# Kernel optimization log

Measured on AMD Instinct MI355X. Metric: run time of the kernel, lower is better.

Reference implementation:

```python
import jax, jax.numpy as jnp
import numpy as np

KF, KD, STRIDE, PAD = 5, 3, 1, 2  # filter width, depth, stride, padding from cfg
N, C, H, W = 256, 3, 224, 224


def setup_inputs() -> dict:
    key = jax.random.key(0)
    k1, k2, k3 = jax.random.split(key, 3)
    bound = 1.0 / np.sqrt(KF * KF * KD)  # nn.Linear default init bound
    x = jax.random.normal(k1, (N, C, H, W), dtype=jnp.float32)
    W_lin = jax.random.uniform(k2, (1, KF * KF * KD), dtype=jnp.float32, minval=-bound, maxval=bound)
    b = jax.random.uniform(k3, (1,), dtype=jnp.float32, minval=-bound, maxval=bound)
    return {"x": x, "W_lin": W_lin, "b": b}


def reference(x, W_lin, b):
    # Linear over patches flattened in (C, Kh, Kw) order == conv with OIHW kernel.
    w = W_lin.reshape(1, KD, KF, KF)  # [O=1, I=3, Kh=5, Kw=5]
    out = jax.lax.conv_general_dilated(
        x, w,
        window_strides=(STRIDE, STRIDE),
        padding=[(PAD, PAD), (PAD, PAD)],
        dimension_numbers=("NCHW", "OIHW", "NCHW"),
    )  # [N, 1, H, W]
    out = out + b  # bias broadcast
    return out[:, 0, :, :]  # module returns [N, W, H] with W == H
```

## Files before the change

### kernel.cpp

```cpp
#include <hip/hip_runtime.h>


namespace {

constexpr int Hc = 224, Wc = 224, Cc = 3;
constexpr int HW = Hc * Wc;
constexpr int CHW = Cc * HW;
constexpr int BAND = 16;
constexpr int SROWS = BAND + 4;
constexpr int RST = 232;
constexpr int BUFD = SROWS * RST;
constexpr int SPI = Hc / BAND;
constexpr int BLK = 256;

__device__ __forceinline__ void gl_lds16(const float* g, float* l) {
  __builtin_amdgcn_global_load_lds(
      (const __attribute__((address_space(1))) void*)g,
      (__attribute__((address_space(3))) void*)l, 16, 0, 0);
}

__global__ __launch_bounds__(BLK) void conv5x5_r21(
    const float* __restrict__ x, const float* __restrict__ wl,
    const float* __restrict__ bptr, float* __restrict__ out) {
  __shared__ __align__(16) float sm[2 * BUFD];

  const int tid = threadIdx.x;
  const int lane = tid & 63;
  const int wv = tid >> 6;

  const int cpx = gridDim.x >> 3;
  const int bid = (blockIdx.x & 7) * cpx + (blockIdx.x >> 3);
  const int n = bid / SPI;
  const int band = bid % SPI;

  float w[Cc][5][5];
#pragma unroll
  for (int c = 0; c < Cc; ++c)
#pragma unroll
    for (int i = 0; i < 25; ++i) w[c][i / 5][i % 5] = wl[c * 25 + i];
  const float bias = bptr[0];

  const float* xn = x + (size_t)n * CHW;
  float* outn = out + (size_t)n * HW;

  const int g = tid & 31;
  const int tg = tid >> 5;
  const bool lo = (g == 0), hi = (g == 31);
  const int rdo = g * 7 + 2;

  float acc[2][7];

#define STAGE_P(P)                                                            \
  do {                                                                        \
    const float* gch_ = xn + (size_t)(P) * HW;                                \
    float* smb_ = sm + ((P) & 1) * BUFD;                                      \
    _Pragma("unroll") for (int i_ = 0; i_ < 5; ++i_) {                        \
      const int r_ = wv + 4 * i_;                                             \
      const int gy_ = band * BAND - 2 + r_;                                   \
      float* ld_ = smb_ + r_ * RST + 4;                                       \
      if (gy_ >= 0 && gy_ < Hc) {                                             \
        if (lane < 56)                                                        \
          gl_lds16(gch_ + (size_t)gy_ * Wc + lane * 4, ld_);                  \
      } else {                                                                \
        if (lane < 56)                                                        \
          *(float4*)(ld_ + lane * 4) = make_float4(0.f, 0.f, 0.f, 0.f);       \
      }                                                                       \
    }                                                                         \
  } while (0)

#define COMPUTE_P(P)                                                          \
  do {                                                                        \
    constexpr int ch_ = (P);                                                  \
    const float* smb_ = sm + ((P) & 1) * BUFD;                                \
    if (ch_ == 0) {                                                           \
      _Pragma("unroll") for (int r_ = 0; r_ < 2; ++r_)                        \
          _Pragma("unroll") for (int c_ = 0; c_ < 7; ++c_)                    \
              acc[r_][c_] = 0.f;                                              \
    }                                                                         \
    _Pragma("unroll") for (int jj_ = 0; jj_ < 6; ++jj_) {                     \
      const float* rp_ = smb_ + (tg * 2 + jj_) * RST + rdo;                   \
      float win_[11];                                                         \
      _Pragma("unroll") for (int j_ = 0; j_ < 11; ++j_) win_[j_] = rp_[j_];   \
      win_[0] = lo ? 0.f : win_[0];                                           \
      win_[1] = lo ? 0.f : win_[1];                                           \
      win_[9] = hi ? 0.f : win_[9];                                           \
      win_[10] = hi ? 0.f : win_[10];                                         \
      _Pragma("unroll") for (int r_ = 0; r_ < 2; ++r_) {                      \
        if (r_ <= jj_ && jj_ - r_ <= 4) {                                     \
          _Pragma("unroll") for (int kx_ = 0; kx_ < 5; ++kx_) {               \
            const float wv_ = w[ch_][jj_ - r_][kx_];                          \
            _Pragma("unroll") for (int c_ = 0; c_ < 7; ++c_) {                \
              acc[r_][c_] = fmaf(win_[c_ + kx_], wv_, acc[r_][c_]);           \
            }                                                                 \
          }                                                                   \
        }                                                                     \
      }                                                                       \
    }                                                                         \
    if (ch_ == 2) {                                                           \
      _Pragma("unroll") for (int r_ = 0; r_ < 2; ++r_) {                      \
        const int gy_ = band * BAND + tg * 2 + r_;                            \
        float* op_ = outn + (size_t)gy_ * Wc + g * 7;                         \
        _Pragma("unroll") for (int c_ = 0; c_ < 7; ++c_)                      \
            op_[c_] = acc[r_][c_] + bias;                                     \
      }                                                                       \
    }                                                                         \
  } while (0)

  STAGE_P(0);
  __syncthreads(); STAGE_P(1); COMPUTE_P(0);
  __syncthreads(); STAGE_P(2); COMPUTE_P(1);
  __syncthreads();             COMPUTE_P(2);

#undef STAGE_P
#undef COMPUTE_P
}

}

extern "C" void kernel_launch(void* const* d_in, const int* in_sizes, int n_in,
                              void* d_out, int out_size, void* d_ws, size_t ws_size,
                              hipStream_t stream) {
  const float* x  = (const float*)d_in[0];
  const float* wl = (const float*)d_in[1];
  const float* b  = (const float*)d_in[2];
  float* out = (float*)d_out;

  const int N = out_size / HW;
  const int nblk = N * SPI;

  conv5x5_r21<<<nblk, BLK, 0, stream>>>(x, wl, b, out);
}
```

Before: 42.54 us.

## Process two bands per block with a six-stage pipeline and pre-zeroed halo

Each block now handles two consecutive 16-row bands, so the double-buffered channel pipeline runs six stages instead of three and is primed once per two bands. Grid size is halved. The left and right halo columns in shared memory are zeroed once up front, which removes the per-window lo/hi selects in the inner loop. Compute sections are wrapped in s_setprio to raise wave priority during the FMAs. The tradeoff is fewer blocks for latency hiding and a dependence on the staging loads never overwriting the zeroed halo columns.

Measured after the change: 47.89 us. 1.13x slower.

```diff
diff --git a/kernel.cpp b/kernel.cpp
--- a/kernel.cpp
+++ b/kernel.cpp
@@ -10,7 +10,7 @@
 constexpr int SROWS = BAND + 4;
 constexpr int RST = 232;
 constexpr int BUFD = SROWS * RST;
-constexpr int SPI = Hc / BAND;
+constexpr int CPI = 7;
 constexpr int BLK = 256;
 
 __device__ __forceinline__ void gl_lds16(const float* g, float* l) {
@@ -19,7 +19,7 @@
       (__attribute__((address_space(3))) void*)l, 16, 0, 0);
 }
 
-__global__ __launch_bounds__(BLK) void conv5x5_r21(
+__global__ __launch_bounds__(BLK) void conv5x5_r23(
     const float* __restrict__ x, const float* __restrict__ wl,
     const float* __restrict__ bptr, float* __restrict__ out) {
   __shared__ __align__(16) float sm[2 * BUFD];
@@ -30,8 +30,8 @@
 
   const int cpx = gridDim.x >> 3;
   const int bid = (blockIdx.x & 7) * cpx + (blockIdx.x >> 3);
-  const int n = bid / SPI;
-  const int band = bid % SPI;
+  const int n = bid / CPI;
+  const int b0 = (bid % CPI) * 2;
 
   float w[Cc][5][5];
 #pragma unroll
@@ -45,18 +45,27 @@
 
   const int g = tid & 31;
   const int tg = tid >> 5;
-  const bool lo = (g == 0), hi = (g == 31);
   const int rdo = g * 7 + 2;
 
   float acc[2][7];
 
+  if (tid < 160) {
+    const int buf = tid / 80;
+    const int rem = tid % 80;
+    const int row = rem >> 2;
+    const int j = rem & 3;
+    const int dw = (j < 2) ? (2 + j) : (226 + j);
+    sm[buf * BUFD + row * RST + dw] = 0.f;
+  }
+
 #define STAGE_P(P)                                                            \
   do {                                                                        \
-    const float* gch_ = xn + (size_t)(P) * HW;                                \
+    const int band_ = b0 + (P) / 3;                                           \
+    const float* gch_ = xn + (size_t)((P) % 3) * HW;                          \
     float* smb_ = sm + ((P) & 1) * BUFD;                                      \
     _Pragma("unroll") for (int i_ = 0; i_ < 5; ++i_) {                        \
       const int r_ = wv + 4 * i_;                                             \
-      const int gy_ = band * BAND - 2 + r_;                                   \
+      const int gy_ = band_ * BAND - 2 + r_;                                  \
       float* ld_ = smb_ + r_ * RST + 4;                                       \
       if (gy_ >= 0 && gy_ < Hc) {                                             \
         if (lane < 56)                                                        \
@@ -70,21 +79,19 @@
 
 #define COMPUTE_P(P)                                                          \
   do {                                                                        \
-    constexpr int ch_ = (P);                                                  \
+    constexpr int ch_ = (P) % 3;                                              \
+    const int band_ = b0 + (P) / 3;                                           \
     const float* smb_ = sm + ((P) & 1) * BUFD;                                \
     if (ch_ == 0) {                                                           \
       _Pragma("unroll") for (int r_ = 0; r_ < 2; ++r_)                        \
           _Pragma("unroll") for (int c_ = 0; c_ < 7; ++c_)                    \
               acc[r_][c_] = 0.f;                                              \
     }                                                                         \
+    __builtin_amdgcn_s_setprio(1);                                            \
     _Pragma("unroll") for (int jj_ = 0; jj_ < 6; ++jj_) {                     \
       const float* rp_ = smb_ + (tg * 2 + jj_) * RST + rdo;                   \
       float win_[11];                                                         \
       _Pragma("unroll") for (int j_ = 0; j_ < 11; ++j_) win_[j_] = rp_[j_];   \
-      win_[0] = lo ? 0.f : win_[0];                                           \
-      win_[1] = lo ? 0.f : win_[1];                                           \
-      win_[9] = hi ? 0.f : win_[9];                                           \
-      win_[10] = hi ? 0.f : win_[10];                                         \
       _Pragma("unroll") for (int r_ = 0; r_ < 2; ++r_) {                      \
         if (r_ <= jj_ && jj_ - r_ <= 4) {                                     \
           _Pragma("unroll") for (int kx_ = 0; kx_ < 5; ++kx_) {               \
@@ -96,9 +103,10 @@
         }                                                                     \
       }                                                                       \
     }                                                                         \
+    __builtin_amdgcn_s_setprio(0);                                            \
     if (ch_ == 2) {                                                           \
       _Pragma("unroll") for (int r_ = 0; r_ < 2; ++r_) {                      \
-        const int gy_ = band * BAND + tg * 2 + r_;                            \
+        const int gy_ = band_ * BAND + tg * 2 + r_;                           \
         float* op_ = outn + (size_t)gy_ * Wc + g * 7;                         \
         _Pragma("unroll") for (int c_ = 0; c_ < 7; ++c_)                      \
             op_[c_] = acc[r_][c_] + bias;                                     \
@@ -109,7 +117,10 @@
   STAGE_P(0);
   __syncthreads(); STAGE_P(1); COMPUTE_P(0);
   __syncthreads(); STAGE_P(2); COMPUTE_P(1);
-  __syncthreads();             COMPUTE_P(2);
+  __syncthreads(); STAGE_P(3); COMPUTE_P(2);
+  __syncthreads(); STAGE_P(4); COMPUTE_P(3);
+  __syncthreads(); STAGE_P(5); COMPUTE_P(4);
+  __syncthreads();             COMPUTE_P(5);
 
 #undef STAGE_P
 #undef COMPUTE_P
@@ -126,7 +137,7 @@
   float* out = (float*)d_out;
 
   const int N = out_size / HW;
-  const int nblk = N * SPI;
+  const int nblk = N * CPI;
 
-  conv5x5_r21<<<nblk, BLK, 0, stream>>>(x, wl, b, out);
+  conv5x5_r23<<<nblk, BLK, 0, stream>>>(x, wl, b, out);
 }
```

## Give each wavefront its own 4-row slice with private LDS buffers, no block barriers

Applied to the files above, without the earlier changes.

Restructures the conv so each 64-lane wavefront owns a 4-output-row slice with a private double-buffered LDS region. Barrier-based staging is replaced by manual vmcnt/lgkmcnt waits, so waves never synchronise with each other. Halo rows are loaded with clamped addresses and then zeroed for edge slices, and the left/right padding columns are zeroed once in LDS instead of per-window selects. Vertical halo overhead rises from 4 extra rows per 16 to 4 per 4, which increases global load traffic, and correctness now depends on hand-written wait counts.

New measurement: 44.38 us. +4.3%, slower.

```diff
diff --git a/kernel.cpp b/kernel.cpp
--- a/kernel.cpp
+++ b/kernel.cpp
@@ -6,12 +6,11 @@
 constexpr int Hc = 224, Wc = 224, Cc = 3;
 constexpr int HW = Hc * Wc;
 constexpr int CHW = Cc * HW;
-constexpr int BAND = 16;
-constexpr int SROWS = BAND + 4;
 constexpr int RST = 232;
-constexpr int BUFD = SROWS * RST;
-constexpr int SPI = Hc / BAND;
-constexpr int BLK = 256;
+constexpr int SR = 8;
+constexpr int BUFD = SR * RST;
+constexpr int BLK = 128;
+constexpr int SLICES = 56;
 
 __device__ __forceinline__ void gl_lds16(const float* g, float* l) {
   __builtin_amdgcn_global_load_lds(
@@ -19,19 +18,22 @@
       (__attribute__((address_space(3))) void*)l, 16, 0, 0);
 }
 
-__global__ __launch_bounds__(BLK) void conv5x5_r21(
+__global__ __launch_bounds__(BLK) void conv5x5_r25(
     const float* __restrict__ x, const float* __restrict__ wl,
     const float* __restrict__ bptr, float* __restrict__ out) {
-  __shared__ __align__(16) float sm[2 * BUFD];
+  __shared__ __align__(16) float sm[2 * 2 * BUFD];
 
   const int tid = threadIdx.x;
   const int lane = tid & 63;
   const int wv = tid >> 6;
+  float* mylds = sm + wv * (2 * BUFD);
 
   const int cpx = gridDim.x >> 3;
   const int bid = (blockIdx.x & 7) * cpx + (blockIdx.x >> 3);
-  const int n = bid / SPI;
-  const int band = bid % SPI;
+  const int sid = bid * 2 + wv;
+  const int n = sid / SLICES;
+  const int slice = sid % SLICES;
+  const int oy0 = slice * 4;
 
   float w[Cc][5][5];
 #pragma unroll
@@ -43,48 +45,63 @@
   const float* xn = x + (size_t)n * CHW;
   float* outn = out + (size_t)n * HW;
 
-  const int g = tid & 31;
-  const int tg = tid >> 5;
-  const bool lo = (g == 0), hi = (g == 31);
+  const int g = lane & 31;
+  const int tg = lane >> 5;
   const int rdo = g * 7 + 2;
 
   float acc[2][7];
 
-#define STAGE_P(P)                                                            \
+  {
+    const int bu = lane >> 5;
+    const int rr = (lane & 31) >> 2;
+    const int j = lane & 3;
+    mylds[bu * BUFD + rr * RST + (j < 2 ? 2 + j : 226 + j)] = 0.f;
+  }
+
+#define STAGE_W(CH, B)                                                        \
   do {                                                                        \
-    const float* gch_ = xn + (size_t)(P) * HW;                                \
-    float* smb_ = sm + ((P) & 1) * BUFD;                                      \
-    _Pragma("unroll") for (int i_ = 0; i_ < 5; ++i_) {                        \
-      const int r_ = wv + 4 * i_;                                             \
-      const int gy_ = band * BAND - 2 + r_;                                   \
-      float* ld_ = smb_ + r_ * RST + 4;                                       \
-      if (gy_ >= 0 && gy_ < Hc) {                                             \
-        if (lane < 56)                                                        \
-          gl_lds16(gch_ + (size_t)gy_ * Wc + lane * 4, ld_);                  \
-      } else {                                                                \
-        if (lane < 56)                                                        \
-          *(float4*)(ld_ + lane * 4) = make_float4(0.f, 0.f, 0.f, 0.f);       \
+    const float* gch_ = xn + (size_t)(CH) * HW;                               \
+    float* dst_ = mylds + (B) * BUFD;                                         \
+    _Pragma("unroll") for (int r_ = 0; r_ < SR; ++r_) {                       \
+      const int gy_ = oy0 - 2 + r_;                                           \
+      const int yc_ = gy_ < 0 ? 0 : (gy_ > Hc - 1 ? Hc - 1 : gy_);            \
+      if (lane < 56)                                                          \
+        gl_lds16(gch_ + (size_t)yc_ * Wc + lane * 4, dst_ + r_ * RST + 4);    \
+    }                                                                         \
+  } while (0)
+
+#define FIX_OOB(B)                                                            \
+  do {                                                                        \
+    if (slice == 0) {                                                         \
+      if (lane < 56) {                                                        \
+        *(float4*)(mylds + (B) * BUFD + 0 * RST + 4 + lane * 4) =             \
+            make_float4(0.f, 0.f, 0.f, 0.f);                                  \
+        *(float4*)(mylds + (B) * BUFD + 1 * RST + 4 + lane * 4) =             \
+            make_float4(0.f, 0.f, 0.f, 0.f);                                  \
+      }                                                                       \
+    } else if (slice == SLICES - 1) {                                         \
+      if (lane < 56) {                                                        \
+        *(float4*)(mylds + (B) * BUFD + 6 * RST + 4 + lane * 4) =             \
+            make_float4(0.f, 0.f, 0.f, 0.f);                                  \
+        *(float4*)(mylds + (B) * BUFD + 7 * RST + 4 + lane * 4) =             \
+            make_float4(0.f, 0.f, 0.f, 0.f);                                  \
       }                                                                       \
     }                                                                         \
   } while (0)
 
-#define COMPUTE_P(P)                                                          \
+#define COMPUTE_W(CH, B)                                                      \
   do {                                                                        \
-    constexpr int ch_ = (P);                                                  \
-    const float* smb_ = sm + ((P) & 1) * BUFD;                                \
+    constexpr int ch_ = (CH);                                                 \
+    const float* bp_ = mylds + (B) * BUFD;                                    \
     if (ch_ == 0) {                                                           \
       _Pragma("unroll") for (int r_ = 0; r_ < 2; ++r_)                        \
           _Pragma("unroll") for (int c_ = 0; c_ < 7; ++c_)                    \
               acc[r_][c_] = 0.f;                                              \
     }                                                                         \
     _Pragma("unroll") for (int jj_ = 0; jj_ < 6; ++jj_) {                     \
-      const float* rp_ = smb_ + (tg * 2 + jj_) * RST + rdo;                   \
+      const float* rp_ = bp_ + (tg * 2 + jj_) * RST + rdo;                    \
       float win_[11];                                                         \
       _Pragma("unroll") for (int j_ = 0; j_ < 11; ++j_) win_[j_] = rp_[j_];   \
-      win_[0] = lo ? 0.f : win_[0];                                           \
-      win_[1] = lo ? 0.f : win_[1];                                           \
-      win_[9] = hi ? 0.f : win_[9];                                           \
-      win_[10] = hi ? 0.f : win_[10];                                         \
       _Pragma("unroll") for (int r_ = 0; r_ < 2; ++r_) {                      \
         if (r_ <= jj_ && jj_ - r_ <= 4) {                                     \
           _Pragma("unroll") for (int kx_ = 0; kx_ < 5; ++kx_) {               \
@@ -98,7 +115,7 @@
     }                                                                         \
     if (ch_ == 2) {                                                           \
       _Pragma("unroll") for (int r_ = 0; r_ < 2; ++r_) {                      \
-        const int gy_ = band * BAND + tg * 2 + r_;                            \
+        const int gy_ = oy0 + tg * 2 + r_;                                    \
         float* op_ = outn + (size_t)gy_ * Wc + g * 7;                         \
         _Pragma("unroll") for (int c_ = 0; c_ < 7; ++c_)                      \
             op_[c_] = acc[r_][c_] + bias;                                     \
@@ -106,13 +123,24 @@
     }                                                                         \
   } while (0)
 
-  STAGE_P(0);
-  __syncthreads(); STAGE_P(1); COMPUTE_P(0);
-  __syncthreads(); STAGE_P(2); COMPUTE_P(1);
-  __syncthreads();             COMPUTE_P(2);
+  STAGE_W(0, 0);
+  STAGE_W(1, 1);
+  asm volatile("s_waitcnt vmcnt(8)" ::: "memory");
+  FIX_OOB(0);
+  COMPUTE_W(0, 0);
+  asm volatile("s_waitcnt lgkmcnt(0)" ::: "memory");
+  __builtin_amdgcn_sched_barrier(0);
+  STAGE_W(2, 0);
+  asm volatile("s_waitcnt vmcnt(8)" ::: "memory");
+  FIX_OOB(1);
+  COMPUTE_W(1, 1);
+  asm volatile("s_waitcnt vmcnt(0)" ::: "memory");
+  FIX_OOB(0);
+  COMPUTE_W(2, 0);
 
-#undef STAGE_P
-#undef COMPUTE_P
+#undef STAGE_W
+#undef FIX_OOB
+#undef COMPUTE_W
 }
 
 }
@@ -126,7 +154,6 @@
   float* out = (float*)d_out;
 
   const int N = out_size / HW;
-  const int nblk = N * SPI;
-
-  conv5x5_r21<<<nblk, BLK, 0, stream>>>(x, wl, b, out);
+  const int nblk = N * SLICES / 2;
+  conv5x5_r25<<<nblk, BLK, 0, stream>>>(x, wl, b, out);
 }
```
